# Kernel optimization log

Hardware: AMD Instinct MI355X
Metric: run time of the kernel (lower is better)

Reference implementation:

```python
import jax, jax.numpy as jnp
import numpy as np

NU, NI, E, NNZ, NLAYERS, TOPK = 2560, 3584, 64, 200000, 2, 5
N = NU + NI
DQK = 4 * E  # Linear(dim, 4*dim)


def setup_inputs() -> dict:
    key = jax.random.key(0)
    ks = jax.random.split(key, 14)
    s = 1.0 / np.sqrt(E)
    return {
        "user_emb": jax.random.normal(ks[0], (NU, E), jnp.float32) * s,
        "item_emb": jax.random.normal(ks[1], (NI, E), jnp.float32) * s,
        "norm_rows": jax.random.randint(ks[2], (NNZ,), 0, N, jnp.int32),
        "norm_cols": jax.random.randint(ks[3], (NNZ,), 0, N, jnp.int32),
        "norm_vals": jax.random.uniform(ks[4], (NNZ,), jnp.float32) / 32.0,
        "adj_rows": jax.random.randint(ks[5], (NNZ,), 0, N, jnp.int32),
        "adj_cols": jax.random.randint(ks[6], (NNZ,), 0, N, jnp.int32),
        "adj_vals": jnp.ones((NNZ,), jnp.float32),
        "Wq": jax.random.normal(ks[7], (DQK, E), jnp.float32) * s,
        "bq": jnp.zeros((DQK,), jnp.float32),
        "Wk": jax.random.normal(ks[8], (DQK, E), jnp.float32) * s,
        "bk": jnp.zeros((DQK,), jnp.float32),
        "Wv": jax.random.normal(ks[9], (DQK, E), jnp.float32) * s,
        "bv": jnp.zeros((DQK,), jnp.float32),
    }


def reference(user_emb, item_emb, norm_rows, norm_cols, norm_vals,
              adj_rows, adj_cols, adj_vals, Wq, bq, Wk, bk, Wv, bv):
    # densified sparse adjacencies (duplicates accumulated, as COO spmm would)
    A_norm = jnp.zeros((N, N), jnp.float32).at[norm_rows, norm_cols].add(norm_vals)
    A = jnp.zeros((N, N), jnp.float32).at[adj_rows, adj_cols].add(adj_vals)

    ego = jnp.concatenate([user_emb, item_emb], axis=0)  # [N, E]
    layers = []
    att_out = None
    for _ in range(NLAYERS):
        layers.append(ego)
        # GNN propagation: sparse.mm(norm_adj, ego)
        ego = A_norm @ ego  # [N, E]
        # dense similarity + sparse-blended similarity
        sim = ego @ ego.T                      # [N, N]
        sim = sim + 0.5 * (A @ sim)            # [N, N]
        # top-K neighbor selection + gather
        _, idx = jax.lax.top_k(sim, TOPK)      # [N, K]
        sample = ego[idx]                      # [N, K, E]
        # SampleAttention: Linear(dim, 4*dim) Q/K/V, scaled dot-product over K neighbors
        q = ego @ Wq.T + bq                    # [N, 4E]
        kk = sample @ Wk.T + bk                # [N, K, 4E]
        vv = sample @ Wv.T + bv                # [N, K, 4E]
        scores = jnp.einsum('nd,nkd->nk', q, kk) / jnp.sqrt(jnp.float32(DQK))
        att = jax.nn.softmax(scores, axis=-1)
        att_out = jnp.einsum('nk,nkd->nd', att, vv)  # [N, 4E]
    mean_emb = jnp.mean(jnp.stack(layers, axis=1), axis=1)  # [N, E]
    return mean_emb[:NU], mean_emb[NU:], att_out
```

## Files before the change

kernel.cpp:

```cpp
#include <hip/hip_runtime.h>
#include <math.h>

#define NUSER 2560
#define NITEM 3584
#define NN    6144
#define EDIM  64
#define NNZ   200000
#define DQK   256
#define KTOP  5
#define SPLITS 8
#define TPS    6
#define CK     8
#define ELLW   96
#define TPB   256
#define QKV_BLOCKS 576
#define TOPK_BLOCKS (96 * SPLITS)
#define BSTR  72

typedef __attribute__((ext_vector_type(8))) short bf16x8;
typedef __attribute__((ext_vector_type(4))) float f32x4;

__device__ __forceinline__ unsigned short f2bf(float f) {
    unsigned int b = __float_as_uint(f);
    unsigned int r = (b + 0x7FFFu + ((b >> 16) & 1u)) >> 16;
    return (unsigned short)r;
}
__device__ __forceinline__ int pack2(float a, float b) {
    return (int)f2bf(a) | ((int)f2bf(b) << 16);
}
__device__ __forceinline__ void ell_unpack(long long v, int* col, float* w) {
    *col = (int)(v & 0xffffffffLL);
    *w   = __int_as_float((int)(v >> 32));
}

__global__ void build_kernel(const int* __restrict__ nr, const int* __restrict__ nc,
                             const float* __restrict__ nv,
                             const int* __restrict__ ar, const int* __restrict__ ac,
                             int* __restrict__ cnt_n, int* __restrict__ cnt_a,
                             long long* __restrict__ cv_n, int* __restrict__ cv_a) {
    int g = blockIdx.x * TPB + threadIdx.x;
    if (g < NNZ) {
        int r = __builtin_nontemporal_load(&nr[g]);
        int c = __builtin_nontemporal_load(&nc[g]);
        float v = __builtin_nontemporal_load(&nv[g]);
        int slot = atomicAdd(&cnt_n[r], 1);
        long long pk = (unsigned int)c | ((long long)(unsigned int)__float_as_int(v) << 32);
        __builtin_nontemporal_store(pk, &cv_n[r * ELLW + slot]);
    } else if (g < 2 * NNZ) {
        int h = g - NNZ;
        int r = __builtin_nontemporal_load(&ar[h]);
        int c = __builtin_nontemporal_load(&ac[h]);
        int slot = atomicAdd(&cnt_a[r], 1);
        __builtin_nontemporal_store(c, &cv_a[r * ELLW + slot]);
    }
}

__global__ __launch_bounds__(TPB) void spmm_ell_emb_kernel(
        const int* __restrict__ cnt, const long long* __restrict__ cv,
        const float* __restrict__ user, const float* __restrict__ item,
        float* __restrict__ dst) {
    int r = blockIdx.x * 4 + (threadIdx.x >> 6);
    int lane = threadIdx.x & 63;
    int s = r * ELLW, e = s + cnt[r];
    float a[8];
#pragma unroll
    for (int u = 0; u < 8; ++u) a[u] = 0.f;
    int j = s, n8 = s + ((e - s) & ~7);
    for (; j < n8; j += 8) {
        int col[8]; float w[8];
#pragma unroll
        for (int u = 0; u < 8; ++u) ell_unpack(__builtin_nontemporal_load(&cv[j + u]), &col[u], &w[u]);
#pragma unroll
        for (int u = 0; u < 8; ++u) {
            float x = (col[u] < NUSER) ? user[col[u] * EDIM + lane]
                                       : item[(col[u] - NUSER) * EDIM + lane];
            a[u] = fmaf(w[u], x, a[u]);
        }
    }
    for (; j < e; ++j) {
        int col; float w;
        ell_unpack(__builtin_nontemporal_load(&cv[j]), &col, &w);
        float x = (col < NUSER) ? user[col * EDIM + lane] : item[(col - NUSER) * EDIM + lane];
        a[0] = fmaf(w, x, a[0]);
    }
    dst[r * EDIM + lane] = ((a[0] + a[1]) + (a[2] + a[3])) + ((a[4] + a[5]) + (a[6] + a[7]));
}

__global__ __launch_bounds__(TPB) void spmm_ell_kernel(
        const int* __restrict__ cnt, const long long* __restrict__ cv,
        const float* __restrict__ src, float* __restrict__ dst) {
    int r = blockIdx.x * 4 + (threadIdx.x >> 6);
    int lane = threadIdx.x & 63;
    int s = r * ELLW, e = s + cnt[r];
    float a[8];
#pragma unroll
    for (int u = 0; u < 8; ++u) a[u] = 0.f;
    int j = s, n8 = s + ((e - s) & ~7);
    for (; j < n8; j += 8) {
        int col[8]; float w[8];
#pragma unroll
        for (int u = 0; u < 8; ++u) ell_unpack(__builtin_nontemporal_load(&cv[j + u]), &col[u], &w[u]);
#pragma unroll
        for (int u = 0; u < 8; ++u)
            a[u] = fmaf(w[u], src[col[u] * EDIM + lane], a[u]);
    }
    for (; j < e; ++j) {
        int col; float w;
        ell_unpack(__builtin_nontemporal_load(&cv[j]), &col, &w);
        a[0] = fmaf(w, src[col * EDIM + lane], a[0]);
    }
    dst[r * EDIM + lane] = ((a[0] + a[1]) + (a[2] + a[3])) + ((a[4] + a[5]) + (a[6] + a[7]));
}

__global__ __launch_bounds__(TPB) void qm_mean_kernel(
        const int* __restrict__ cnt, const int* __restrict__ cv,
        const float* __restrict__ ego2, const float* __restrict__ ego1,
        const float* __restrict__ user, const float* __restrict__ item,
        float* __restrict__ Qm, float* __restrict__ outmean) {
    int r = blockIdx.x * 4 + (threadIdx.x >> 6);
    int lane = threadIdx.x & 63;
    int s = r * ELLW, e = s + cnt[r];
    float a[8];
#pragma unroll
    for (int u = 0; u < 8; ++u) a[u] = 0.f;
    int j = s, n8 = s + ((e - s) & ~7);
    for (; j < n8; j += 8) {
        int col[8];
#pragma unroll
        for (int u = 0; u < 8; ++u) col[u] = __builtin_nontemporal_load(&cv[j + u]);
#pragma unroll
        for (int u = 0; u < 8; ++u)
            a[u] += ego2[col[u] * EDIM + lane];
    }
    for (; j < e; ++j) {
        int col = __builtin_nontemporal_load(&cv[j]);
        a[0] += ego2[col * EDIM + lane];
    }
    float acc = ((a[0] + a[1]) + (a[2] + a[3])) + ((a[4] + a[5]) + (a[6] + a[7]));
    int o = r * EDIM + lane;
    Qm[o] = ego2[o] + 0.5f * acc;
    float e0v = (r < NUSER) ? user[o] : item[o - NUSER * EDIM];
    outmean[o] = 0.5f * (e0v + ego1[o]);
}

__device__ __forceinline__ void ins3(float v, int ci, float tv[3], int ti[3]) {
    if (v > tv[2]) {
        bool p1 = v > tv[1], p0 = v > tv[0];
        tv[2] = p1 ? tv[1] : v;  ti[2] = p1 ? ti[1] : ci;
        if (p1) { tv[1] = p0 ? tv[0] : v; ti[1] = p0 ? ti[0] : ci; }
        if (p0) { tv[0] = v; ti[0] = ci; }
    }
}

__global__ __launch_bounds__(TPB, 3) void qkv_topk_kernel(
        const float* __restrict__ ego2,
        const float* __restrict__ Wq, const float* __restrict__ bq,
        const float* __restrict__ Wk, const float* __restrict__ bk,
        const float* __restrict__ Wv, const float* __restrict__ bv,
        float* __restrict__ Qa, float* __restrict__ Ka, float* __restrict__ Va,
        const float* __restrict__ Qm,
        int* __restrict__ pidx) {
    __shared__ __align__(16) float smem[12288];
    int t = threadIdx.x;

    if (blockIdx.x < QKV_BLOCKS) {
        int tx = t & 15, ty = t >> 4;
        int id = blockIdx.x;
        int bz = id / 192, rem = id % 192, by = rem / 96, bx = rem % 96;
        const float* W; const float* b; float* out;
        if (bz == 0)      { W = Wq; b = bq; out = Qa; }
        else if (bz == 1) { W = Wk; b = bk; out = Ka; }
        else              { W = Wv; b = bv; out = Va; }
        float* As = smem;
        float* Bs = smem + 4096;
        int r0 = bx * 64, d0 = by * 128;
        {
            int r = t & 63, eb = (t >> 6) * 16;
#pragma unroll
            for (int rep = 0; rep < 4; ++rep) {
                int e0 = eb + rep * 4;
                float4 v = *(const float4*)&ego2[(r0 + r) * EDIM + e0];
                As[(e0 + 0) * 64 + r] = v.x; As[(e0 + 1) * 64 + r] = v.y;
                As[(e0 + 2) * 64 + r] = v.z; As[(e0 + 3) * 64 + r] = v.w;
            }
        }
        {
            int d = t & 127, eb = (t >> 7) * 32;
#pragma unroll
            for (int rep = 0; rep < 8; ++rep) {
                int e0 = eb + rep * 4;
                float4 v = *(const float4*)&W[(d0 + d) * EDIM + e0];
                Bs[(e0 + 0) * 128 + d] = v.x; Bs[(e0 + 1) * 128 + d] = v.y;
                Bs[(e0 + 2) * 128 + d] = v.z; Bs[(e0 + 3) * 128 + d] = v.w;
            }
        }
        __syncthreads();
        float acc[4][8];
#pragma unroll
        for (int i = 0; i < 4; ++i)
#pragma unroll
            for (int j = 0; j < 8; ++j) acc[i][j] = 0.f;
#pragma unroll 4
        for (int e = 0; e < 64; ++e) {
            float4 a  = *(const float4*)&As[e * 64 + ty * 4];
            float4 b0 = *(const float4*)&Bs[e * 128 + tx * 4];
            float4 b1 = *(const float4*)&Bs[e * 128 + 64 + tx * 4];
            float ar[4] = {a.x, a.y, a.z, a.w};
#pragma unroll
            for (int i = 0; i < 4; ++i) {
                acc[i][0] = fmaf(ar[i], b0.x, acc[i][0]);
                acc[i][1] = fmaf(ar[i], b0.y, acc[i][1]);
                acc[i][2] = fmaf(ar[i], b0.z, acc[i][2]);
                acc[i][3] = fmaf(ar[i], b0.w, acc[i][3]);
                acc[i][4] = fmaf(ar[i], b1.x, acc[i][4]);
                acc[i][5] = fmaf(ar[i], b1.y, acc[i][5]);
                acc[i][6] = fmaf(ar[i], b1.z, acc[i][6]);
                acc[i][7] = fmaf(ar[i], b1.w, acc[i][7]);
            }
        }
        float4 bias0 = *(const float4*)&b[d0 + tx * 4];
        float4 bias1 = *(const float4*)&b[d0 + 64 + tx * 4];
#pragma unroll
        for (int i = 0; i < 4; ++i) {
            int r = r0 + ty * 4 + i;
            float4 o0 = make_float4(acc[i][0] + bias0.x, acc[i][1] + bias0.y,
                                    acc[i][2] + bias0.z, acc[i][3] + bias0.w);
            float4 o1 = make_float4(acc[i][4] + bias1.x, acc[i][5] + bias1.y,
                                    acc[i][6] + bias1.z, acc[i][7] + bias1.w);
            *(float4*)&out[r * DQK + d0 + tx * 4] = o0;
            *(float4*)&out[r * DQK + d0 + 64 + tx * 4] = o1;
        }
        return;
    }

    int id = blockIdx.x - QKV_BLOCKS;
    int rb = id % 96, sp = id / 96;
    int r0 = rb * 64;
    int w = t >> 6, lane = t & 63, lq = lane >> 4, lc = lane & 15;

    short* Ah = (short*)smem;
    short* Bh = Ah + 64 * EDIM;

    {
        int row = t >> 2, seg = t & 3;
        const float4* src = (const float4*)&Qm[(size_t)(r0 + row) * EDIM + seg * 16];
        float4 f0 = src[0], f1 = src[1], f2 = src[2], f3 = src[3];
        int4 p0, p1;
        p0.x = pack2(f0.x, f0.y); p0.y = pack2(f0.z, f0.w);
        p0.z = pack2(f1.x, f1.y); p0.w = pack2(f1.z, f1.w);
        p1.x = pack2(f2.x, f2.y); p1.y = pack2(f2.z, f2.w);
        p1.z = pack2(f3.x, f3.y); p1.w = pack2(f3.z, f3.w);
        *(int4*)&Ah[row * EDIM + seg * 16] = p0;
        *(int4*)&Ah[row * EDIM + seg * 16 + 8] = p1;
    }

    float4 pa[4], pb[4];
    {
        int c0 = (sp * TPS) * 128;
#pragma unroll
        for (int rep = 0; rep < 4; ++rep) {
            int v = t + 256 * rep;
            const float4* src = (const float4*)&ego2[(size_t)(c0 + (v >> 3)) * EDIM + (v & 7) * 8];
            pa[rep] = src[0]; pb[rep] = src[1];
        }
    }

    float t3v[4][3]; int t3i[4][3];
#pragma unroll
    for (int i = 0; i < 4; ++i)
#pragma unroll
        for (int k = 0; k < 3; ++k) { t3v[i][k] = -INFINITY; t3i[i][k] = 0x7fffffff; }

    bf16x8 af0, af1;
    for (int tile = 0; tile < TPS; ++tile) {
        int c0 = (sp * TPS + tile) * 128;
        __syncthreads();
        {
#pragma unroll
            for (int rep = 0; rep < 4; ++rep) {
                int v = t + 256 * rep;
                int4 q;
                q.x = pack2(pa[rep].x, pa[rep].y); q.y = pack2(pa[rep].z, pa[rep].w);
                q.z = pack2(pb[rep].x, pb[rep].y); q.w = pack2(pb[rep].z, pb[rep].w);
                *(int4*)&Bh[(v >> 3) * BSTR + (v & 7) * 8] = q;
            }
        }
        if (tile + 1 < TPS) {
            int c1 = c0 + 128;
#pragma unroll
            for (int rep = 0; rep < 4; ++rep) {
                int v = t + 256 * rep;
                const float4* src = (const float4*)&ego2[(size_t)(c1 + (v >> 3)) * EDIM + (v & 7) * 8];
                pa[rep] = src[0]; pb[rep] = src[1];
            }
        }
        __syncthreads();
        if (tile == 0) {
            af0 = *(const bf16x8*)&Ah[(w * 16 + lc) * EDIM + lq * 8];
            af1 = *(const bf16x8*)&Ah[(w * 16 + lc) * EDIM + 32 + lq * 8];
        }

#pragma unroll
        for (int ch = 0; ch < 8; ++ch) {
            bf16x8 b0 = *(const bf16x8*)&Bh[(ch * 16 + lc) * BSTR + lq * 8];
            bf16x8 b1 = *(const bf16x8*)&Bh[(ch * 16 + lc) * BSTR + 32 + lq * 8];
            f32x4 acc = {0.f, 0.f, 0.f, 0.f};
            acc = __builtin_amdgcn_mfma_f32_16x16x32_bf16(af0, b0, acc, 0, 0, 0);
            acc = __builtin_amdgcn_mfma_f32_16x16x32_bf16(af1, b1, acc, 0, 0, 0);
            int ci = c0 + ch * 16 + lc;
#pragma unroll
            for (int reg = 0; reg < 4; ++reg)
                ins3(acc[reg], ci, t3v[reg], t3i[reg]);
        }
    }

#pragma unroll
    for (int i = 0; i < 4; ++i) {
        int row = r0 + w * 16 + lq * 4 + i;
        int ptr = 0;
        for (int k = 0; k < CK; ++k) {
            float cvv = (ptr == 0) ? t3v[i][0] : (ptr == 1) ? t3v[i][1]
                      : (ptr == 2) ? t3v[i][2] : -INFINITY;
            int   cii = (ptr == 0) ? t3i[i][0] : (ptr == 1) ? t3i[i][1]
                      : (ptr == 2) ? t3i[i][2] : 0x7fffffff;
            float bv = cvv; int bi = cii;
#pragma unroll
            for (int off = 1; off < 16; off <<= 1) {
                float ov = __shfl_xor(bv, off, 64);
                int   oi = __shfl_xor(bi, off, 64);
                if (ov > bv || (ov == bv && oi < bi)) { bv = ov; bi = oi; }
            }
            if (bv == cvv && bi == cii) ptr++;
            if (lc == 0) pidx[(row * SPLITS + sp) * CK + k] = bi;
        }
    }
}

__global__ __launch_bounds__(TPB) void attn_kernel(
        const float* __restrict__ Qm, const float* __restrict__ ego2,
        const float* __restrict__ Qa, const float* __restrict__ Ka, const float* __restrict__ Va,
        const int* __restrict__ pidx, float* __restrict__ out) {
    __shared__ float sb[4][64];
    int wv = threadIdx.x >> 6, lane = threadIdx.x & 63;
    int r = blockIdx.x * 4 + wv;
    int ci0 = pidx[r * (SPLITS * CK) + lane];
    int part = lane & 3;

    const float4* qmp = (const float4*)(Qm + (size_t)r * EDIM + part * 16);
    float4 q0 = qmp[0], q1 = qmp[1], q2 = qmp[2], q3 = qmp[3];

#pragma unroll
    for (int p = 0; p < 4; ++p) {
        int j = p * 16 + (lane >> 2);
        int c = __shfl(ci0, j, 64);
        const float4* ep = (const float4*)(ego2 + (size_t)c * EDIM + part * 16);
        float4 e0 = ep[0], e1 = ep[1], e2 = ep[2], e3 = ep[3];
        float s = 0.f;
        s = fmaf(q0.x, e0.x, s); s = fmaf(q0.y, e0.y, s); s = fmaf(q0.z, e0.z, s); s = fmaf(q0.w, e0.w, s);
        s = fmaf(q1.x, e1.x, s); s = fmaf(q1.y, e1.y, s); s = fmaf(q1.z, e1.z, s); s = fmaf(q1.w, e1.w, s);
        s = fmaf(q2.x, e2.x, s); s = fmaf(q2.y, e2.y, s); s = fmaf(q2.z, e2.z, s); s = fmaf(q2.w, e2.w, s);
        s = fmaf(q3.x, e3.x, s); s = fmaf(q3.y, e3.y, s); s = fmaf(q3.z, e3.z, s); s = fmaf(q3.w, e3.w, s);
        s += __shfl_xor(s, 1, 64);
        s += __shfl_xor(s, 2, 64);
        if (part == 0) sb[wv][j] = s;
    }
    float sv = sb[wv][lane];

    float prevv = INFINITY; int previ = -1;
    int cI[KTOP];
#pragma unroll
    for (int k = 0; k < KTOP; ++k) {
        bool adm = (sv < prevv) || (sv == prevv && ci0 > previ);
        float bv = adm ? sv : -INFINITY;
        int   bi = adm ? ci0 : 0x7fffffff;
#pragma unroll
        for (int off = 1; off < 64; off <<= 1) {
            float ov = __shfl_xor(bv, off, 64);
            int   oi = __shfl_xor(bi, off, 64);
            if (ov > bv || (ov == bv && oi < bi)) { bv = ov; bi = oi; }
        }
        cI[k] = bi; prevv = bv; previ = bi;
    }

    float4 q = *(const float4*)&Qa[r * DQK + lane * 4];
    float sc[KTOP];
#pragma unroll
    for (int k = 0; k < KTOP; ++k) {
        float4 kk = *(const float4*)&Ka[cI[k] * DQK + lane * 4];
        float p = q.x * kk.x + q.y * kk.y + q.z * kk.z + q.w * kk.w;
#pragma unroll
        for (int off = 32; off; off >>= 1) p += __shfl_xor(p, off, 64);
        sc[k] = p * 0.0625f;
    }
    float m = sc[0];
#pragma unroll
    for (int k = 1; k < KTOP; ++k) m = fmaxf(m, sc[k]);
    float wgt[KTOP], ssum = 0.f;
#pragma unroll
    for (int k = 0; k < KTOP; ++k) { wgt[k] = expf(sc[k] - m); ssum += wgt[k]; }
    float inv = 1.f / ssum;
    float4 o = make_float4(0.f, 0.f, 0.f, 0.f);
#pragma unroll
    for (int k = 0; k < KTOP; ++k) {
        float4 vv = *(const float4*)&Va[cI[k] * DQK + lane * 4];
        float a = wgt[k] * inv;
        o.x = fmaf(a, vv.x, o.x); o.y = fmaf(a, vv.y, o.y);
        o.z = fmaf(a, vv.z, o.z); o.w = fmaf(a, vv.w, o.w);
    }
    *(float4*)&out[r * DQK + lane * 4] = o;
}

extern "C" void kernel_launch(void* const* d_in, const int* in_sizes, int n_in,
                              void* d_out, int out_size, void* d_ws, size_t ws_size,
                              hipStream_t stream) {
    const float* user  = (const float*)d_in[0];
    const float* item  = (const float*)d_in[1];
    const int*   nrows = (const int*)d_in[2];
    const int*   ncols = (const int*)d_in[3];
    const float* nvals = (const float*)d_in[4];
    const int*   arows = (const int*)d_in[5];
    const int*   acols = (const int*)d_in[6];
    const float* Wq = (const float*)d_in[8];  const float* bq = (const float*)d_in[9];
    const float* Wk = (const float*)d_in[10]; const float* bk = (const float*)d_in[11];
    const float* Wv = (const float*)d_in[12]; const float* bv = (const float*)d_in[13];
    float* out = (float*)d_out;
    float* ws  = (float*)d_ws;

    const int NE  = NN * EDIM;
    const int NQK = NN * DQK;
    float* ego1 = ws;
    float* ego2 = ws + NE;
    float* Qm   = ws + 2 * NE;
    float* Qa   = ws + 3 * NE;
    float* Ka   = Qa + NQK;
    float* Va   = Ka + NQK;
    int*   pidx = (int*)(Va + NQK);

    int* ell    = (int*)Qa;
    int* cnt_n  = ell;
    int* cnt_a  = ell + 6144;
    long long* cv_n = (long long*)(ell + 12288);
    int* cv_a   = (int*)(cv_n + NN * ELLW);

    hipMemsetAsync(cnt_n, 0, 12288 * sizeof(int), stream);
    build_kernel<<<(2 * NNZ + TPB - 1) / TPB, TPB, 0, stream>>>(nrows, ncols, nvals,
                                                                arows, acols,
                                                                cnt_n, cnt_a, cv_n, cv_a);
    spmm_ell_emb_kernel<<<NN / 4, TPB, 0, stream>>>(cnt_n, cv_n, user, item, ego1);
    spmm_ell_kernel<<<NN / 4, TPB, 0, stream>>>(cnt_n, cv_n, ego1, ego2);
    qm_mean_kernel<<<NN / 4, TPB, 0, stream>>>(cnt_a, cv_a, ego2, ego1, user, item, Qm, out);
    qkv_topk_kernel<<<QKV_BLOCKS + TOPK_BLOCKS, TPB, 0, stream>>>(
        ego2, Wq, bq, Wk, bk, Wv, bv, Qa, Ka, Va, Qm, pidx);
    attn_kernel<<<NN / 4, TPB, 0, stream>>>(Qm, ego2, Qa, Ka, Va, pidx, out + NE);
}
```

Baseline: 204.0 us.

## Fold Q/K projections into 64x64 Gram matrix and apply V after attention

The Q·K attention scores are computed algebraically as ego·(Wq^T Wk)·sample + bq·Wk·sample. A 64x64 Gram matrix is built in an extra block of the build kernel, and a per-row projected vector P is formed in extra blocks of qm_mean. The full N×256 Q/K/V projections are no longer materialized. Attention weights mix 64-dim ego rows, and a single GEMM with Wv at the end produces the 256-dim output, using the fact that the softmax weights sum to one so the bias is preserved. Nontemporal loads and stores are also dropped. The cost is a small serial Gram computation and different floating-point rounding.

```diff
diff --git a/kernel.cpp b/kernel.cpp
--- a/kernel.cpp
+++ b/kernel.cpp
@@ -13,8 +13,7 @@
 #define CK     8
 #define ELLW   96
 #define TPB   256
-#define QKV_BLOCKS 576
-#define TOPK_BLOCKS (96 * SPLITS)
+#define NBUILD 1563
 #define BSTR  72
 
 typedef __attribute__((ext_vector_type(8))) short bf16x8;
@@ -36,22 +35,68 @@
 __global__ void build_kernel(const int* __restrict__ nr, const int* __restrict__ nc,
                              const float* __restrict__ nv,
                              const int* __restrict__ ar, const int* __restrict__ ac,
+                             const float* __restrict__ Wq, const float* __restrict__ Wk,
+                             const float* __restrict__ bq,
                              int* __restrict__ cnt_n, int* __restrict__ cnt_a,
-                             long long* __restrict__ cv_n, int* __restrict__ cv_a) {
-    int g = blockIdx.x * TPB + threadIdx.x;
+                             long long* __restrict__ cv_n, int* __restrict__ cv_a,
+                             float* __restrict__ Gbuf) {
+    __shared__ float gq[4096];
+    __shared__ float gk[4096];
+    int t = threadIdx.x;
+
+    if (blockIdx.x == NBUILD) {
+        float accG[16];
+#pragma unroll
+        for (int i = 0; i < 16; ++i) accG[i] = 0.f;
+        float uacc = 0.f;
+        int e = t >> 2, fb = (t & 3) * 16;
+        for (int d0 = 0; d0 < DQK; d0 += 64) {
+            __syncthreads();
+#pragma unroll
+            for (int i = 0; i < 16; ++i) {
+                int v = i * 256 + t;
+                gq[v] = Wq[d0 * 64 + v];
+                gk[v] = Wk[d0 * 64 + v];
+            }
+            __syncthreads();
+            for (int dc = 0; dc < 64; ++dc) {
+                float a = gq[dc * 64 + e];
+                float4 w0 = *(const float4*)&gk[dc * 64 + fb];
+                float4 w1 = *(const float4*)&gk[dc * 64 + fb + 4];
+                float4 w2 = *(const float4*)&gk[dc * 64 + fb + 8];
+                float4 w3 = *(const float4*)&gk[dc * 64 + fb + 12];
+                accG[0]  = fmaf(a, w0.x, accG[0]);  accG[1]  = fmaf(a, w0.y, accG[1]);
+                accG[2]  = fmaf(a, w0.z, accG[2]);  accG[3]  = fmaf(a, w0.w, accG[3]);
+                accG[4]  = fmaf(a, w1.x, accG[4]);  accG[5]  = fmaf(a, w1.y, accG[5]);
+                accG[6]  = fmaf(a, w1.z, accG[6]);  accG[7]  = fmaf(a, w1.w, accG[7]);
+                accG[8]  = fmaf(a, w2.x, accG[8]);  accG[9]  = fmaf(a, w2.y, accG[9]);
+                accG[10] = fmaf(a, w2.z, accG[10]); accG[11] = fmaf(a, w2.w, accG[11]);
+                accG[12] = fmaf(a, w3.x, accG[12]); accG[13] = fmaf(a, w3.y, accG[13]);
+                accG[14] = fmaf(a, w3.z, accG[14]); accG[15] = fmaf(a, w3.w, accG[15]);
+            }
+            if (t < 64) {
+                for (int dc = 0; dc < 64; ++dc)
+                    uacc = fmaf(bq[d0 + dc], gk[dc * 64 + t], uacc);
+            }
+        }
+#pragma unroll
+        for (int i = 0; i < 16; ++i) Gbuf[e * 64 + fb + i] = accG[i];
+        if (t < 64) Gbuf[4096 + t] = uacc;
+        return;
+    }
+
+    int g = blockIdx.x * TPB + t;
     if (g < NNZ) {
-        int r = __builtin_nontemporal_load(&nr[g]);
-        int c = __builtin_nontemporal_load(&nc[g]);
-        float v = __builtin_nontemporal_load(&nv[g]);
+        int r = nr[g], c = nc[g];
+        float v = nv[g];
         int slot = atomicAdd(&cnt_n[r], 1);
         long long pk = (unsigned int)c | ((long long)(unsigned int)__float_as_int(v) << 32);
-        __builtin_nontemporal_store(pk, &cv_n[r * ELLW + slot]);
+        cv_n[r * ELLW + slot] = pk;
     } else if (g < 2 * NNZ) {
         int h = g - NNZ;
-        int r = __builtin_nontemporal_load(&ar[h]);
-        int c = __builtin_nontemporal_load(&ac[h]);
+        int r = ar[h], c = ac[h];
         int slot = atomicAdd(&cnt_a[r], 1);
-        __builtin_nontemporal_store(c, &cv_a[r * ELLW + slot]);
+        cv_a[r * ELLW + slot] = c;
     }
 }
 
@@ -69,7 +114,7 @@
     for (; j < n8; j += 8) {
         int col[8]; float w[8];
 #pragma unroll
-        for (int u = 0; u < 8; ++u) ell_unpack(__builtin_nontemporal_load(&cv[j + u]), &col[u], &w[u]);
+        for (int u = 0; u < 8; ++u) ell_unpack(cv[j + u], &col[u], &w[u]);
 #pragma unroll
         for (int u = 0; u < 8; ++u) {
             float x = (col[u] < NUSER) ? user[col[u] * EDIM + lane]
@@ -79,7 +124,7 @@
     }
     for (; j < e; ++j) {
         int col; float w;
-        ell_unpack(__builtin_nontemporal_load(&cv[j]), &col, &w);
+        ell_unpack(cv[j], &col, &w);
         float x = (col < NUSER) ? user[col * EDIM + lane] : item[(col - NUSER) * EDIM + lane];
         a[0] = fmaf(w, x, a[0]);
     }
@@ -99,14 +144,14 @@
     for (; j < n8; j += 8) {
         int col[8]; float w[8];
 #pragma unroll
-        for (int u = 0; u < 8; ++u) ell_unpack(__builtin_nontemporal_load(&cv[j + u]), &col[u], &w[u]);
+        for (int u = 0; u < 8; ++u) ell_unpack(cv[j + u], &col[u], &w[u]);
 #pragma unroll
         for (int u = 0; u < 8; ++u)
             a[u] = fmaf(w[u], src[col[u] * EDIM + lane], a[u]);
     }
     for (; j < e; ++j) {
         int col; float w;
-        ell_unpack(__builtin_nontemporal_load(&cv[j]), &col, &w);
+        ell_unpack(cv[j], &col, &w);
         a[0] = fmaf(w, src[col * EDIM + lane], a[0]);
     }
     dst[r * EDIM + lane] = ((a[0] + a[1]) + (a[2] + a[3])) + ((a[4] + a[5]) + (a[6] + a[7]));
@@ -116,9 +161,56 @@
         const int* __restrict__ cnt, const int* __restrict__ cv,
         const float* __restrict__ ego2, const float* __restrict__ ego1,
         const float* __restrict__ user, const float* __restrict__ item,
-        float* __restrict__ Qm, float* __restrict__ outmean) {
-    int r = blockIdx.x * 4 + (threadIdx.x >> 6);
-    int lane = threadIdx.x & 63;
+        const float* __restrict__ Gbuf,
+        float* __restrict__ Qm, float* __restrict__ outmean, float* __restrict__ P) {
+    __shared__ float Gs[4160];
+    int t = threadIdx.x;
+
+    if (blockIdx.x >= NN / 4) {
+        int pb = blockIdx.x - NN / 4;
+#pragma unroll
+        for (int i = 0; i < 17; ++i) {
+            int v = i * 256 + t;
+            if (v < 4160) Gs[v] = Gbuf[v];
+        }
+        __syncthreads();
+        int r = pb * 64 + (t >> 2), fb = (t & 3) * 16;
+        const float4* row4 = (const float4*)(ego2 + (size_t)r * EDIM);
+        float4 rw[16];
+#pragma unroll
+        for (int i = 0; i < 16; ++i) rw[i] = row4[i];
+        float4 acc0 = *(const float4*)&Gs[4096 + fb];
+        float4 acc1 = *(const float4*)&Gs[4096 + fb + 4];
+        float4 acc2 = *(const float4*)&Gs[4096 + fb + 8];
+        float4 acc3 = *(const float4*)&Gs[4096 + fb + 12];
+#pragma unroll
+        for (int ee = 0; ee < 16; ++ee) {
+            float av[4] = {rw[ee].x, rw[ee].y, rw[ee].z, rw[ee].w};
+#pragma unroll
+            for (int q = 0; q < 4; ++q) {
+                int e = ee * 4 + q;
+                float a = av[q];
+                float4 g0 = *(const float4*)&Gs[e * 64 + fb];
+                float4 g1 = *(const float4*)&Gs[e * 64 + fb + 4];
+                float4 g2 = *(const float4*)&Gs[e * 64 + fb + 8];
+                float4 g3 = *(const float4*)&Gs[e * 64 + fb + 12];
+                acc0.x = fmaf(a, g0.x, acc0.x); acc0.y = fmaf(a, g0.y, acc0.y);
+                acc0.z = fmaf(a, g0.z, acc0.z); acc0.w = fmaf(a, g0.w, acc0.w);
+                acc1.x = fmaf(a, g1.x, acc1.x); acc1.y = fmaf(a, g1.y, acc1.y);
+                acc1.z = fmaf(a, g1.z, acc1.z); acc1.w = fmaf(a, g1.w, acc1.w);
+                acc2.x = fmaf(a, g2.x, acc2.x); acc2.y = fmaf(a, g2.y, acc2.y);
+                acc2.z = fmaf(a, g2.z, acc2.z); acc2.w = fmaf(a, g2.w, acc2.w);
+                acc3.x = fmaf(a, g3.x, acc3.x); acc3.y = fmaf(a, g3.y, acc3.y);
+                acc3.z = fmaf(a, g3.z, acc3.z); acc3.w = fmaf(a, g3.w, acc3.w);
+            }
+        }
+        float4* dst = (float4*)(P + (size_t)r * EDIM + fb);
+        dst[0] = acc0; dst[1] = acc1; dst[2] = acc2; dst[3] = acc3;
+        return;
+    }
+
+    int r = blockIdx.x * 4 + (t >> 6);
+    int lane = t & 63;
     int s = r * ELLW, e = s + cnt[r];
     float a[8];
 #pragma unroll
@@ -127,15 +219,12 @@
     for (; j < n8; j += 8) {
         int col[8];
 #pragma unroll
-        for (int u = 0; u < 8; ++u) col[u] = __builtin_nontemporal_load(&cv[j + u]);
+        for (int u = 0; u < 8; ++u) col[u] = cv[j + u];
 #pragma unroll
         for (int u = 0; u < 8; ++u)
             a[u] += ego2[col[u] * EDIM + lane];
     }
-    for (; j < e; ++j) {
-        int col = __builtin_nontemporal_load(&cv[j]);
-        a[0] += ego2[col * EDIM + lane];
-    }
+    for (; j < e; ++j) a[0] += ego2[cv[j] * EDIM + lane];
     float acc = ((a[0] + a[1]) + (a[2] + a[3])) + ((a[4] + a[5]) + (a[6] + a[7]));
     int o = r * EDIM + lane;
     Qm[o] = ego2[o] + 0.5f * acc;
@@ -152,94 +241,17 @@
     }
 }
 
-__global__ __launch_bounds__(TPB, 3) void qkv_topk_kernel(
-        const float* __restrict__ ego2,
-        const float* __restrict__ Wq, const float* __restrict__ bq,
-        const float* __restrict__ Wk, const float* __restrict__ bk,
-        const float* __restrict__ Wv, const float* __restrict__ bv,
-        float* __restrict__ Qa, float* __restrict__ Ka, float* __restrict__ Va,
-        const float* __restrict__ Qm,
+__global__ __launch_bounds__(TPB, 6) void topk_kernel(
+        const float* __restrict__ ego2, const float* __restrict__ Qm,
         int* __restrict__ pidx) {
-    __shared__ __align__(16) float smem[12288];
+    __shared__ __align__(16) short smem[13312];
     int t = threadIdx.x;
-
-    if (blockIdx.x < QKV_BLOCKS) {
-        int tx = t & 15, ty = t >> 4;
-        int id = blockIdx.x;
-        int bz = id / 192, rem = id % 192, by = rem / 96, bx = rem % 96;
-        const float* W; const float* b; float* out;
-        if (bz == 0)      { W = Wq; b = bq; out = Qa; }
-        else if (bz == 1) { W = Wk; b = bk; out = Ka; }
-        else              { W = Wv; b = bv; out = Va; }
-        float* As = smem;
-        float* Bs = smem + 4096;
-        int r0 = bx * 64, d0 = by * 128;
-        {
-            int r = t & 63, eb = (t >> 6) * 16;
-#pragma unroll
-            for (int rep = 0; rep < 4; ++rep) {
-                int e0 = eb + rep * 4;
-                float4 v = *(const float4*)&ego2[(r0 + r) * EDIM + e0];
-                As[(e0 + 0) * 64 + r] = v.x; As[(e0 + 1) * 64 + r] = v.y;
-                As[(e0 + 2) * 64 + r] = v.z; As[(e0 + 3) * 64 + r] = v.w;
-            }
-        }
-        {
-            int d = t & 127, eb = (t >> 7) * 32;
-#pragma unroll
-            for (int rep = 0; rep < 8; ++rep) {
-                int e0 = eb + rep * 4;
-                float4 v = *(const float4*)&W[(d0 + d) * EDIM + e0];
-                Bs[(e0 + 0) * 128 + d] = v.x; Bs[(e0 + 1) * 128 + d] = v.y;
-                Bs[(e0 + 2) * 128 + d] = v.z; Bs[(e0 + 3) * 128 + d] = v.w;
-            }
-        }
-        __syncthreads();
-        float acc[4][8];
-#pragma unroll
-        for (int i = 0; i < 4; ++i)
-#pragma unroll
-            for (int j = 0; j < 8; ++j) acc[i][j] = 0.f;
-#pragma unroll 4
-        for (int e = 0; e < 64; ++e) {
-            float4 a  = *(const float4*)&As[e * 64 + ty * 4];
-            float4 b0 = *(const float4*)&Bs[e * 128 + tx * 4];
-            float4 b1 = *(const float4*)&Bs[e * 128 + 64 + tx * 4];
-            float ar[4] = {a.x, a.y, a.z, a.w};
-#pragma unroll
-            for (int i = 0; i < 4; ++i) {
-                acc[i][0] = fmaf(ar[i], b0.x, acc[i][0]);
-                acc[i][1] = fmaf(ar[i], b0.y, acc[i][1]);
-                acc[i][2] = fmaf(ar[i], b0.z, acc[i][2]);
-                acc[i][3] = fmaf(ar[i], b0.w, acc[i][3]);
-                acc[i][4] = fmaf(ar[i], b1.x, acc[i][4]);
-                acc[i][5] = fmaf(ar[i], b1.y, acc[i][5]);
-                acc[i][6] = fmaf(ar[i], b1.z, acc[i][6]);
-                acc[i][7] = fmaf(ar[i], b1.w, acc[i][7]);
-            }
-        }
-        float4 bias0 = *(const float4*)&b[d0 + tx * 4];
-        float4 bias1 = *(const float4*)&b[d0 + 64 + tx * 4];
-#pragma unroll
-        for (int i = 0; i < 4; ++i) {
-            int r = r0 + ty * 4 + i;
-            float4 o0 = make_float4(acc[i][0] + bias0.x, acc[i][1] + bias0.y,
-                                    acc[i][2] + bias0.z, acc[i][3] + bias0.w);
-            float4 o1 = make_float4(acc[i][4] + bias1.x, acc[i][5] + bias1.y,
-                                    acc[i][6] + bias1.z, acc[i][7] + bias1.w);
-            *(float4*)&out[r * DQK + d0 + tx * 4] = o0;
-            *(float4*)&out[r * DQK + d0 + 64 + tx * 4] = o1;
-        }
-        return;
-    }
-
-    int id = blockIdx.x - QKV_BLOCKS;
-    int rb = id % 96, sp = id / 96;
+    int rb = blockIdx.x % 96, sp = blockIdx.x / 96;
     int r0 = rb * 64;
     int w = t >> 6, lane = t & 63, lq = lane >> 4, lc = lane & 15;
 
-    short* Ah = (short*)smem;
-    short* Bh = Ah + 64 * EDIM;
+    short* Ah = smem;
+    short* Bh = smem + 4096;
 
     {
         int row = t >> 2, seg = t & 3;
@@ -336,18 +348,21 @@
     }
 }
 
-__global__ __launch_bounds__(TPB) void attn_kernel(
-        const float* __restrict__ Qm, const float* __restrict__ ego2,
-        const float* __restrict__ Qa, const float* __restrict__ Ka, const float* __restrict__ Va,
-        const int* __restrict__ pidx, float* __restrict__ out) {
+__global__ __launch_bounds__(TPB) void attn_sel_kernel(
+        const float* __restrict__ Qm, const float* __restrict__ P,
+        const float* __restrict__ ego2, const int* __restrict__ pidx,
+        float* __restrict__ m) {
     __shared__ float sb[4][64];
+    __shared__ float sa[4][64];
     int wv = threadIdx.x >> 6, lane = threadIdx.x & 63;
     int r = blockIdx.x * 4 + wv;
-    int ci0 = pidx[r * (SPLITS * CK) + lane];
+    int ci0 = pidx[r * 64 + lane];
     int part = lane & 3;
 
     const float4* qmp = (const float4*)(Qm + (size_t)r * EDIM + part * 16);
     float4 q0 = qmp[0], q1 = qmp[1], q2 = qmp[2], q3 = qmp[3];
+    const float4* pmp = (const float4*)(P + (size_t)r * EDIM + part * 16);
+    float4 p0 = pmp[0], p1 = pmp[1], p2 = pmp[2], p3 = pmp[3];
 
 #pragma unroll
     for (int p = 0; p < 4; ++p) {
@@ -355,59 +370,122 @@
         int c = __shfl(ci0, j, 64);
         const float4* ep = (const float4*)(ego2 + (size_t)c * EDIM + part * 16);
         float4 e0 = ep[0], e1 = ep[1], e2 = ep[2], e3 = ep[3];
-        float s = 0.f;
+        float s = 0.f, s2 = 0.f;
         s = fmaf(q0.x, e0.x, s); s = fmaf(q0.y, e0.y, s); s = fmaf(q0.z, e0.z, s); s = fmaf(q0.w, e0.w, s);
         s = fmaf(q1.x, e1.x, s); s = fmaf(q1.y, e1.y, s); s = fmaf(q1.z, e1.z, s); s = fmaf(q1.w, e1.w, s);
         s = fmaf(q2.x, e2.x, s); s = fmaf(q2.y, e2.y, s); s = fmaf(q2.z, e2.z, s); s = fmaf(q2.w, e2.w, s);
         s = fmaf(q3.x, e3.x, s); s = fmaf(q3.y, e3.y, s); s = fmaf(q3.z, e3.z, s); s = fmaf(q3.w, e3.w, s);
-        s += __shfl_xor(s, 1, 64);
-        s += __shfl_xor(s, 2, 64);
-        if (part == 0) sb[wv][j] = s;
+        s2 = fmaf(p0.x, e0.x, s2); s2 = fmaf(p0.y, e0.y, s2); s2 = fmaf(p0.z, e0.z, s2); s2 = fmaf(p0.w, e0.w, s2);
+        s2 = fmaf(p1.x, e1.x, s2); s2 = fmaf(p1.y, e1.y, s2); s2 = fmaf(p1.z, e1.z, s2); s2 = fmaf(p1.w, e1.w, s2);
+        s2 = fmaf(p2.x, e2.x, s2); s2 = fmaf(p2.y, e2.y, s2); s2 = fmaf(p2.z, e2.z, s2); s2 = fmaf(p2.w, e2.w, s2);
+        s2 = fmaf(p3.x, e3.x, s2); s2 = fmaf(p3.y, e3.y, s2); s2 = fmaf(p3.z, e3.z, s2); s2 = fmaf(p3.w, e3.w, s2);
+        s  += __shfl_xor(s, 1, 64);  s  += __shfl_xor(s, 2, 64);
+        s2 += __shfl_xor(s2, 1, 64); s2 += __shfl_xor(s2, 2, 64);
+        if (part == 0) { sb[wv][j] = s; sa[wv][j] = s2; }
     }
     float sv = sb[wv][lane];
+    float av = sa[wv][lane];
 
     float prevv = INFINITY; int previ = -1;
-    int cI[KTOP];
+    int cI[KTOP]; float atk[KTOP];
 #pragma unroll
     for (int k = 0; k < KTOP; ++k) {
         bool adm = (sv < prevv) || (sv == prevv && ci0 > previ);
         float bv = adm ? sv : -INFINITY;
         int   bi = adm ? ci0 : 0x7fffffff;
+        float ba = av;
 #pragma unroll
         for (int off = 1; off < 64; off <<= 1) {
             float ov = __shfl_xor(bv, off, 64);
             int   oi = __shfl_xor(bi, off, 64);
-            if (ov > bv || (ov == bv && oi < bi)) { bv = ov; bi = oi; }
-        }
-        cI[k] = bi; prevv = bv; previ = bi;
-    }
-
-    float4 q = *(const float4*)&Qa[r * DQK + lane * 4];
+            float oa = __shfl_xor(ba, off, 64);
+            if (ov > bv || (ov == bv && oi < bi)) { bv = ov; bi = oi; ba = oa; }
+        }
+        cI[k] = bi; atk[k] = ba; prevv = bv; previ = bi;
+    }
+
     float sc[KTOP];
 #pragma unroll
-    for (int k = 0; k < KTOP; ++k) {
-        float4 kk = *(const float4*)&Ka[cI[k] * DQK + lane * 4];
-        float p = q.x * kk.x + q.y * kk.y + q.z * kk.z + q.w * kk.w;
-#pragma unroll
-        for (int off = 32; off; off >>= 1) p += __shfl_xor(p, off, 64);
-        sc[k] = p * 0.0625f;
-    }
-    float m = sc[0];
-#pragma unroll
-    for (int k = 1; k < KTOP; ++k) m = fmaxf(m, sc[k]);
+    for (int k = 0; k < KTOP; ++k) sc[k] = atk[k] * 0.0625f;
+    float mx = sc[0];
+#pragma unroll
+    for (int k = 1; k < KTOP; ++k) mx = fmaxf(mx, sc[k]);
     float wgt[KTOP], ssum = 0.f;
 #pragma unroll
-    for (int k = 0; k < KTOP; ++k) { wgt[k] = expf(sc[k] - m); ssum += wgt[k]; }
+    for (int k = 0; k < KTOP; ++k) { wgt[k] = expf(sc[k] - mx); ssum += wgt[k]; }
     float inv = 1.f / ssum;
-    float4 o = make_float4(0.f, 0.f, 0.f, 0.f);
-#pragma unroll
-    for (int k = 0; k < KTOP; ++k) {
-        float4 vv = *(const float4*)&Va[cI[k] * DQK + lane * 4];
-        float a = wgt[k] * inv;
-        o.x = fmaf(a, vv.x, o.x); o.y = fmaf(a, vv.y, o.y);
-        o.z = fmaf(a, vv.z, o.z); o.w = fmaf(a, vv.w, o.w);
-    }
-    *(float4*)&out[r * DQK + lane * 4] = o;
+
+    float mm = 0.f;
+#pragma unroll
+    for (int k = 0; k < KTOP; ++k)
+        mm = fmaf(wgt[k] * inv, ego2[(size_t)cI[k] * EDIM + lane], mm);
+    m[(size_t)r * EDIM + lane] = mm;
+}
+
+__global__ __launch_bounds__(TPB, 3) void gemm_kernel(
+        const float* __restrict__ A, const float* __restrict__ W,
+        const float* __restrict__ b, float* __restrict__ out) {
+    __shared__ __align__(16) float smem[64 * 64 + 128 * 64];
+    float* As = smem;
+    float* Bs = smem + 4096;
+    int t = threadIdx.x, tx = t & 15, ty = t >> 4;
+    int r0 = blockIdx.x * 64, d0 = blockIdx.y * 128;
+    {
+        int r = t & 63, eb = (t >> 6) * 16;
+#pragma unroll
+        for (int rep = 0; rep < 4; ++rep) {
+            int e0 = eb + rep * 4;
+            float4 v = *(const float4*)&A[(r0 + r) * EDIM + e0];
+            As[(e0 + 0) * 64 + r] = v.x; As[(e0 + 1) * 64 + r] = v.y;
+            As[(e0 + 2) * 64 + r] = v.z; As[(e0 + 3) * 64 + r] = v.w;
+        }
+    }
+    {
+        int d = t & 127, eb = (t >> 7) * 32;
+#pragma unroll
+        for (int rep = 0; rep < 8; ++rep) {
+            int e0 = eb + rep * 4;
+            float4 v = *(const float4*)&W[(d0 + d) * EDIM + e0];
+            Bs[(e0 + 0) * 128 + d] = v.x; Bs[(e0 + 1) * 128 + d] = v.y;
+            Bs[(e0 + 2) * 128 + d] = v.z; Bs[(e0 + 3) * 128 + d] = v.w;
+        }
+    }
+    __syncthreads();
+    float acc[4][8];
+#pragma unroll
+    for (int i = 0; i < 4; ++i)
+#pragma unroll
+        for (int j = 0; j < 8; ++j) acc[i][j] = 0.f;
+#pragma unroll 4
+    for (int e = 0; e < 64; ++e) {
+        float4 a  = *(const float4*)&As[e * 64 + ty * 4];
+        float4 b0 = *(const float4*)&Bs[e * 128 + tx * 4];
+        float4 b1 = *(const float4*)&Bs[e * 128 + 64 + tx * 4];
+        float ar[4] = {a.x, a.y, a.z, a.w};
+#pragma unroll
+        for (int i = 0; i < 4; ++i) {
+            acc[i][0] = fmaf(ar[i], b0.x, acc[i][0]);
+            acc[i][1] = fmaf(ar[i], b0.y, acc[i][1]);
+            acc[i][2] = fmaf(ar[i], b0.z, acc[i][2]);
+            acc[i][3] = fmaf(ar[i], b0.w, acc[i][3]);
+            acc[i][4] = fmaf(ar[i], b1.x, acc[i][4]);
+            acc[i][5] = fmaf(ar[i], b1.y, acc[i][5]);
+            acc[i][6] = fmaf(ar[i], b1.z, acc[i][6]);
+            acc[i][7] = fmaf(ar[i], b1.w, acc[i][7]);
+        }
+    }
+    float4 bias0 = *(const float4*)&b[d0 + tx * 4];
+    float4 bias1 = *(const float4*)&b[d0 + 64 + tx * 4];
+#pragma unroll
+    for (int i = 0; i < 4; ++i) {
+        int r = r0 + ty * 4 + i;
+        float4 o0 = make_float4(acc[i][0] + bias0.x, acc[i][1] + bias0.y,
+                                acc[i][2] + bias0.z, acc[i][3] + bias0.w);
+        float4 o1 = make_float4(acc[i][4] + bias1.x, acc[i][5] + bias1.y,
+                                acc[i][6] + bias1.z, acc[i][7] + bias1.w);
+        *(float4*)&out[r * DQK + d0 + tx * 4] = o0;
+        *(float4*)&out[r * DQK + d0 + 64 + tx * 4] = o1;
+    }
 }
 
 extern "C" void kernel_launch(void* const* d_in, const int* in_sizes, int n_in,
@@ -421,35 +499,34 @@
     const int*   arows = (const int*)d_in[5];
     const int*   acols = (const int*)d_in[6];
     const float* Wq = (const float*)d_in[8];  const float* bq = (const float*)d_in[9];
-    const float* Wk = (const float*)d_in[10]; const float* bk = (const float*)d_in[11];
+    const float* Wk = (const float*)d_in[10];
     const float* Wv = (const float*)d_in[12]; const float* bv = (const float*)d_in[13];
     float* out = (float*)d_out;
     float* ws  = (float*)d_ws;
 
-    const int NE  = NN * EDIM;
-    const int NQK = NN * DQK;
+    const int NE = NN * EDIM;
     float* ego1 = ws;
     float* ego2 = ws + NE;
     float* Qm   = ws + 2 * NE;
-    float* Qa   = ws + 3 * NE;
-    float* Ka   = Qa + NQK;
-    float* Va   = Ka + NQK;
-    int*   pidx = (int*)(Va + NQK);
-
-    int* ell    = (int*)Qa;
+    float* P    = ws + 3 * NE;
+    float* m    = ws + 4 * NE;
+    int*   pidx = (int*)(ws + 5 * NE);
+    float* Gbuf = ws + 6 * NE;
+    int*   ell  = (int*)(ws + 6 * NE + 4160);
     int* cnt_n  = ell;
     int* cnt_a  = ell + 6144;
     long long* cv_n = (long long*)(ell + 12288);
     int* cv_a   = (int*)(cv_n + NN * ELLW);
 
     hipMemsetAsync(cnt_n, 0, 12288 * sizeof(int), stream);
-    build_kernel<<<(2 * NNZ + TPB - 1) / TPB, TPB, 0, stream>>>(nrows, ncols, nvals,
-                                                                arows, acols,
-                                                                cnt_n, cnt_a, cv_n, cv_a);
+    build_kernel<<<NBUILD + 1, TPB, 0, stream>>>(nrows, ncols, nvals, arows, acols,
+                                                 Wq, Wk, bq,
+                                                 cnt_n, cnt_a, cv_n, cv_a, Gbuf);
     spmm_ell_emb_kernel<<<NN / 4, TPB, 0, stream>>>(cnt_n, cv_n, user, item, ego1);
     spmm_ell_kernel<<<NN / 4, TPB, 0, stream>>>(cnt_n, cv_n, ego1, ego2);
-    qm_mean_kernel<<<NN / 4, TPB, 0, stream>>>(cnt_a, cv_a, ego2, ego1, user, item, Qm, out);
-    qkv_topk_kernel<<<QKV_BLOCKS + TOPK_BLOCKS, TPB, 0, stream>>>(
-        ego2, Wq, bq, Wk, bk, Wv, bv, Qa, Ka, Va, Qm, pidx);
-    attn_kernel<<<NN / 4, TPB, 0, stream>>>(Qm, ego2, Qa, Ka, Va, pidx, out + NE);
-}
+    qm_mean_kernel<<<NN / 4 + 96, TPB, 0, stream>>>(cnt_a, cv_a, ego2, ego1, user, item,
+                                                    Gbuf, Qm, out, P);
+    topk_kernel<<<96 * SPLITS, TPB, 0, stream>>>(ego2, Qm, pidx);
+    attn_sel_kernel<<<NN / 4, TPB, 0, stream>>>(Qm, P, ego2, pidx, m);
+    gemm_kernel<<<dim3(NN / 64, DQK / 128), TPB, 0, stream>>>(m, Wv, bv, out + NE);
+}
```

Result: slower. 230.2 us (+12.8%).
